# Optimization experiments

Measured on AMD Instinct MI355X. Metric: run time of the kernel, lower is better.

## Reference

```python
import jax, jax.numpy as jnp
import numpy as np

N_NODES = 100000
N_EDGES = 1600000
NEG_SLOPE = 0.2  # PyG GATConv default


def _gat_layer(x, src, dst, W, a_src, a_dst, b, heads, concat):
    """One PyG-style GATConv (eval mode, self-loops already appended)."""
    N = x.shape[0]
    xp = (x @ W).reshape(N, heads, -1)                      # [N, H, C]
    al_s = jnp.einsum('nhc,hc->nh', xp, a_src)              # [N, H]
    al_d = jnp.einsum('nhc,hc->nh', xp, a_dst)              # [N, H]
    e = jax.nn.leaky_relu(al_s[src] + al_d[dst], NEG_SLOPE)  # [E, H]
    # numerically stable segment softmax over incoming edges of each dst
    m = jax.ops.segment_max(e, dst, num_segments=N)         # [N, H]
    ex = jnp.exp(e - m[dst])
    s = jax.ops.segment_sum(ex, dst, num_segments=N)
    alpha = ex / (s[dst] + 1e-16)                           # [E, H]
    out = jax.ops.segment_sum(xp[src] * alpha[:, :, None], dst, num_segments=N)  # [N, H, C]
    out = out.reshape(N, -1) if concat else out.mean(axis=1)
    return out + b


def setup_inputs() -> dict:
    key = jax.random.key(0)
    ks = jax.random.split(key, 16)
    H, C0 = 4, 32  # hidden layers: 4 heads x 32 = 128
    inp = {
        'x': jax.random.normal(ks[0], (N_NODES, 128), dtype=jnp.float32),
        'edge_index': jax.random.randint(ks[1], (2, N_EDGES), 0, N_NODES, dtype=jnp.int64),
        'W0': jax.random.normal(ks[2], (128, 128), dtype=jnp.float32) * 0.1,
        'a_src0': jax.random.normal(ks[3], (H, C0), dtype=jnp.float32) * 0.1,
        'a_dst0': jax.random.normal(ks[4], (H, C0), dtype=jnp.float32) * 0.1,
        'b0': jnp.zeros((128,), dtype=jnp.float32),
        'W1': jax.random.normal(ks[5], (128, 128), dtype=jnp.float32) * 0.1,
        'a_src1': jax.random.normal(ks[6], (H, C0), dtype=jnp.float32) * 0.1,
        'a_dst1': jax.random.normal(ks[7], (H, C0), dtype=jnp.float32) * 0.1,
        'b1': jnp.zeros((128,), dtype=jnp.float32),
        'W2': jax.random.normal(ks[8], (128, 64), dtype=jnp.float32) * 0.1,
        'a_src2': jax.random.normal(ks[9], (1, 64), dtype=jnp.float32) * 0.1,
        'a_dst2': jax.random.normal(ks[10], (1, 64), dtype=jnp.float32) * 0.1,
        'b2': jnp.zeros((64,), dtype=jnp.float32),
    }
    return inp


def reference(x, edge_index, W0, a_src0, a_dst0, b0, W1, a_src1, a_dst1, b1, W2, a_src2, a_dst2, b2):
    N = x.shape[0]
    loop = jnp.arange(N, dtype=edge_index.dtype)
    src = jnp.concatenate([edge_index[0], loop])  # add_self_loops=True
    dst = jnp.concatenate([edge_index[1], loop])
    h = _gat_layer(x, src, dst, W0, a_src0, a_dst0, b0, heads=4, concat=True)
    h = jax.nn.elu(h)
    h = _gat_layer(h, src, dst, W1, a_src1, a_dst1, b1, heads=4, concat=True)
    h = jax.nn.elu(h)
    out = _gat_layer(h, src, dst, W2, a_src2, a_dst2, b2, heads=1, concat=False)
    return out
```

## Files before the change

kernel.cpp:

```cpp
#include <hip/hip_runtime.h>
#include <math.h>


#define N_NODES 100000
#define NBUCK ((N_NODES + 255) / 256)
#define WT_ELEMS (16384 + 16384 + 8192)
#define WT_TOT (WT_ELEMS + NBUCK)

typedef __attribute__((ext_vector_type(4))) _Float16 half4;
typedef __attribute__((ext_vector_type(8))) _Float16 half8;
typedef __attribute__((ext_vector_type(4))) float f32x4;

__device__ inline void fmamix2(float& alo, float& ahi, float s, unsigned u) {
    asm("v_fma_mix_f32 %0, %1, %2, %0 op_sel_hi:[0,1,0]" : "+v"(alo) : "v"(s), "v"(u));
    asm("v_fma_mix_f32 %0, %1, %2, %0 op_sel:[0,1,0] op_sel_hi:[0,1,0]" : "+v"(ahi) : "v"(s), "v"(u));
}


__global__ __launch_bounds__(256) void k_bcount(const int* __restrict__ ei, int E, int ETOT,
                                                int* __restrict__ bucketCnt) {
    __shared__ int h[NBUCK];
    for (int b = threadIdx.x; b < NBUCK; b += 256) h[b] = 0;
    __syncthreads();
    const int base = blockIdx.x * 4096;
#pragma unroll
    for (int j = 0; j < 16; ++j) {
        int idx = base + j * 256 + threadIdx.x;
        if (idx < ETOT) {
            int dst = (idx < E) ? ei[E + idx] : (idx - E);
            atomicAdd(&h[dst >> 8], 1);
        }
    }
    __syncthreads();
    for (int b = threadIdx.x; b < NBUCK; b += 256)
        if (h[b]) atomicAdd(&bucketCnt[b], h[b]);
}

__global__ __launch_bounds__(256) void k_bscan(const int* __restrict__ bucketCnt,
                                               int* __restrict__ bstart,
                                               int* __restrict__ gcur, int ETOT) {
    __shared__ int lds[512];
    const int t = threadIdx.x;
    lds[t] = (t < NBUCK) ? bucketCnt[t] : 0;
    lds[t + 256] = (t + 256 < NBUCK) ? bucketCnt[t + 256] : 0;
    __syncthreads();
    for (int d = 1; d < 512; d <<= 1) {
        int v0 = (t >= d) ? lds[t - d] : 0;
        int v1 = (t + 256 >= d) ? lds[t + 256 - d] : 0;
        __syncthreads();
        lds[t] += v0;
        lds[t + 256] += v1;
        __syncthreads();
    }
    int e0 = (t == 0) ? 0 : lds[t - 1];
    int e1 = lds[t + 255];
    if (t < NBUCK)       { bstart[t] = e0;       gcur[t] = e0; }
    if (t + 256 < NBUCK) { bstart[t + 256] = e1; gcur[t + 256] = e1; }
    if (t == 0) bstart[NBUCK] = ETOT;
}

__global__ __launch_bounds__(256) void k_bplace(const int* __restrict__ ei, int E, int ETOT,
                                                int* __restrict__ gcur, int* __restrict__ tmp) {
    __shared__ int h[NBUCK];
    __shared__ int cur[NBUCK];
    for (int b = threadIdx.x; b < NBUCK; b += 256) h[b] = 0;
    __syncthreads();
    const int base = blockIdx.x * 4096;
    int pk[16], bk[16];
#pragma unroll
    for (int j = 0; j < 16; ++j) {
        int idx = base + j * 256 + threadIdx.x;
        bk[j] = -1;
        if (idx < ETOT) {
            int s, d;
            if (idx < E) { s = ei[idx]; d = ei[E + idx]; }
            else         { s = idx - E; d = idx - E; }
            bk[j] = d >> 8;
            pk[j] = s | ((d & 255) << 17);
            atomicAdd(&h[bk[j]], 1);
        }
    }
    __syncthreads();
    for (int b = threadIdx.x; b < NBUCK; b += 256)
        cur[b] = h[b] ? atomicAdd(&gcur[b], h[b]) : 0;
    __syncthreads();
#pragma unroll
    for (int j = 0; j < 16; ++j) {
        if (bk[j] >= 0) {
            int pos = atomicAdd(&cur[bk[j]], 1);
            tmp[pos] = pk[j];
        }
    }
}

__global__ __launch_bounds__(256) void k_bfinal(const int* __restrict__ tmp,
                                                const int* __restrict__ bstart,
                                                int* __restrict__ rowptr,
                                                int* __restrict__ ssrc, int N) {
    __shared__ int cnt[256];
    __shared__ int cur[256];
    const int t = threadIdx.x;
    const int b = blockIdx.x;
    const int s0 = bstart[b], s1 = bstart[b + 1];
    cnt[t] = 0;
    __syncthreads();
    for (int e = s0 + t; e < s1; e += 256)
        atomicAdd(&cnt[tmp[e] >> 17], 1);
    __syncthreads();
    int c0 = cnt[t];
    for (int d = 1; d < 256; d <<= 1) {
        int v = (t >= d) ? cnt[t - d] : 0;
        __syncthreads();
        cnt[t] += v;
        __syncthreads();
    }
    int excl = cnt[t] - c0;
    int node = b * 256 + t;
    if (node <= N) rowptr[node] = s0 + excl;
    cur[t] = excl;
    __syncthreads();
    for (int e = s0 + t; e < s1; e += 256) {
        int p = tmp[e];
        int pos = atomicAdd(&cur[p >> 17], 1);
        ssrc[s0 + pos] = p & 0x1FFFF;
    }
}

__global__ void k_wt3(const float* __restrict__ W0, const float* __restrict__ W1,
                      const float* __restrict__ W2, _Float16* __restrict__ wt0,
                      _Float16* __restrict__ wt1, _Float16* __restrict__ wt2,
                      int* __restrict__ bucketCnt) {
    int idx = blockIdx.x * 256 + threadIdx.x;
    if (idx < 16384) {
        int k = idx >> 7, n = idx & 127;
        wt0[n * 128 + k] = (_Float16)W0[idx];
    } else if (idx < 32768) {
        int i = idx - 16384;
        int k = i >> 7, n = i & 127;
        wt1[n * 128 + k] = (_Float16)W1[i];
    } else if (idx < WT_ELEMS) {
        int i = idx - 32768;
        int k = i >> 6, n = i & 63;
        wt2[n * 128 + k] = (_Float16)W2[i];
    } else if (idx < WT_TOT) {
        bucketCnt[idx - WT_ELEMS] = 0;
    }
}

template <int OUT, int H, bool INF16>
__global__ __launch_bounds__(256) void k_gemm(const void* __restrict__ Xv_,
                                              const _Float16* __restrict__ Wt,
                                              const float* __restrict__ a_src,
                                              const float* __restrict__ a_dst,
                                              _Float16* __restrict__ XP,
                                              float* __restrict__ al_s,
                                              float* __restrict__ al_d, int N) {
    constexpr int NT = OUT / 16;
    constexpr int C = OUT / H;
    constexpr int LDH = 136;
    __shared__ _Float16 As[64 * LDH];
    __shared__ _Float16 Ws[OUT * LDH];
    const int tid = threadIdx.x;
    const int row0 = blockIdx.x * 64;

    for (int c = tid; c < OUT * 16; c += 256) {
        int r = c >> 4, kc = c & 15;
        *(half8*)&Ws[r * LDH + kc * 8] = *(const half8*)(Wt + r * 128 + kc * 8);
    }
    for (int c = tid; c < 64 * 16; c += 256) {
        int r = c >> 4, kc = c & 15;
        int grow = row0 + r;
        half8 hv;
        if (grow < N) {
            if constexpr (INF16) {
                hv = *(const half8*)((const _Float16*)Xv_ + (size_t)grow * 128 + kc * 8);
            } else {
                const float4* xr = (const float4*)((const float*)Xv_ + (size_t)grow * 128 + kc * 8);
                float4 x0 = xr[0], x1 = xr[1];
                hv[0] = (_Float16)x0.x; hv[1] = (_Float16)x0.y;
                hv[2] = (_Float16)x0.z; hv[3] = (_Float16)x0.w;
                hv[4] = (_Float16)x1.x; hv[5] = (_Float16)x1.y;
                hv[6] = (_Float16)x1.z; hv[7] = (_Float16)x1.w;
            }
        } else {
#pragma unroll
            for (int j = 0; j < 8; ++j) hv[j] = (_Float16)0.f;
        }
        *(half8*)&As[r * LDH + kc * 8] = hv;
    }
    __syncthreads();

    const int w = tid >> 6;
    const int l = tid & 63;
    const int lm = l & 15;
    const int lk = l >> 4;

    f32x4 acc[NT];
#pragma unroll
    for (int nt = 0; nt < NT; ++nt) acc[nt] = {0.f, 0.f, 0.f, 0.f};

#pragma unroll
    for (int ks = 0; ks < 4; ++ks) {
        half8 av = *(const half8*)&As[(w * 16 + lm) * LDH + ks * 32 + lk * 8];
#pragma unroll
        for (int nt = 0; nt < NT; ++nt) {
            half8 bv = *(const half8*)&Ws[(nt * 16 + lm) * LDH + ks * 32 + lk * 8];
            acc[nt] = __builtin_amdgcn_mfma_f32_16x16x32_f16(av, bv, acc[nt], 0, 0, 0);
        }
    }

    float avs[NT], avd[NT];
#pragma unroll
    for (int nt = 0; nt < NT; ++nt) {
        avs[nt] = a_src[nt * 16 + lm];
        avd[nt] = a_dst[nt * 16 + lm];
    }

#pragma unroll
    for (int r = 0; r < 4; ++r) {
        int grow = row0 + w * 16 + lk * 4 + r;
        bool ok = grow < N;
#pragma unroll
        for (int nt = 0; nt < NT; ++nt)
            if (ok) XP[(size_t)grow * OUT + nt * 16 + lm] = (_Float16)acc[nt][r];

        float ps[H], pd[H];
#pragma unroll
        for (int h = 0; h < H; ++h) { ps[h] = 0.f; pd[h] = 0.f; }
#pragma unroll
        for (int nt = 0; nt < NT; ++nt) {
            int h = (nt * 16) / C;
            ps[h] += acc[nt][r] * avs[nt];
            pd[h] += acc[nt][r] * avd[nt];
        }
#pragma unroll
        for (int h = 0; h < H; ++h) {
#pragma unroll
            for (int o = 8; o >= 1; o >>= 1) {
                ps[h] += __shfl_xor(ps[h], o);
                pd[h] += __shfl_xor(pd[h], o);
            }
        }
        if (ok && lm == 0) {
#pragma unroll
            for (int h = 0; h < H; ++h) {
                al_s[(size_t)grow * H + h] = ps[h];
                al_d[(size_t)grow * H + h] = pd[h];
            }
        }
    }
}

template <int OUT, int H, bool ELU, bool OUTF16>
__global__ __launch_bounds__(256) void k_agg(const _Float16* __restrict__ xp,
                                             const float* __restrict__ al_s,
                                             const float* __restrict__ al_d,
                                             const int* __restrict__ rowptr,
                                             const int* __restrict__ ssrc,
                                             const float* __restrict__ bias,
                                             void* __restrict__ out_, int N) {
    constexpr int C = OUT / H;
    constexpr int CPL = OUT / 16;
    const int wid = threadIdx.x >> 6;
    const int lane = threadIdx.x & 63;
    const int qid = lane >> 4;
    const int l4 = lane & 15;
    const int node = blockIdx.x * 4 + wid;
    if (node >= N) return;
    const int rs = rowptr[node];
    const int re = rowptr[node + 1];

    const int c0 = l4 * CPL;
    const int hd = c0 / C;
    const float adh = al_d[(unsigned)node * H + hd];

    float ssum = 0.f;
    float acc[CPL];
#pragma unroll
    for (int j = 0; j < CPL; ++j) acc[j] = 0.f;

    auto edge = [&](int idx) {
        int s = ssrc[idx];
        float e = al_s[(unsigned)s * H + hd] + adh;
        e = e > 0.f ? e : 0.2f * e;
        float a = __expf(e);
        ssum += a;
        unsigned off = (unsigned)s * OUT + c0;
        if constexpr (CPL == 8) {
            uint4 u = *(const uint4*)(xp + off);
            fmamix2(acc[0], acc[1], a, u.x);
            fmamix2(acc[2], acc[3], a, u.y);
            fmamix2(acc[4], acc[5], a, u.z);
            fmamix2(acc[6], acc[7], a, u.w);
        } else {
            uint2 u = *(const uint2*)(xp + off);
            fmamix2(acc[0], acc[1], a, u.x);
            fmamix2(acc[2], acc[3], a, u.y);
        }
    };

    int i = rs;
    for (; i + 16 <= re; i += 16) {
        edge(i + qid); edge(i + qid + 4); edge(i + qid + 8); edge(i + qid + 12);
    }
    for (; i + 8 <= re; i += 8) {
        edge(i + qid); edge(i + qid + 4);
    }
    for (; i + qid < re; i += 4) {
        edge(i + qid);
    }

    ssum += __shfl_xor(ssum, 16);
    ssum += __shfl_xor(ssum, 32);
#pragma unroll
    for (int j = 0; j < CPL; ++j) {
        acc[j] += __shfl_xor(acc[j], 16);
        acc[j] += __shfl_xor(acc[j], 32);
    }

    if (qid == 0) {
        float inv = 1.f / (ssum + 1e-16f);
        float o[CPL];
#pragma unroll
        for (int j = 0; j < CPL; ++j) {
            o[j] = acc[j] * inv + bias[c0 + j];
            if constexpr (ELU) o[j] = o[j] > 0.f ? o[j] : (__expf(o[j]) - 1.f);
        }
        if constexpr (OUTF16) {
            _Float16* op = (_Float16*)out_ + (size_t)node * OUT + c0;
            if constexpr (CPL == 8) {
                half8 hv;
#pragma unroll
                for (int j = 0; j < 8; ++j) hv[j] = (_Float16)o[j];
                *(half8*)op = hv;
            } else {
                half4 hv;
#pragma unroll
                for (int j = 0; j < 4; ++j) hv[j] = (_Float16)o[j];
                *(half4*)op = hv;
            }
        } else {
            float* op = (float*)out_ + (size_t)node * OUT + c0;
            if constexpr (CPL == 8) {
                *(float4*)op = make_float4(o[0], o[1], o[2], o[3]);
                *(float4*)(op + 4) = make_float4(o[4], o[5], o[6], o[7]);
            } else {
                *(float4*)op = make_float4(o[0], o[1], o[2], o[3]);
            }
        }
    }
}


extern "C" void kernel_launch(void* const* d_in, const int* in_sizes, int n_in,
                              void* d_out, int out_size, void* d_ws, size_t ws_size,
                              hipStream_t stream) {
    const int N = N_NODES;
    const float* x     = (const float*)d_in[0];
    const int*   ei    = (const int*)d_in[1];
    const float* W0    = (const float*)d_in[2];
    const float* as0   = (const float*)d_in[3];
    const float* ad0   = (const float*)d_in[4];
    const float* b0    = (const float*)d_in[5];
    const float* W1    = (const float*)d_in[6];
    const float* as1   = (const float*)d_in[7];
    const float* ad1   = (const float*)d_in[8];
    const float* b1    = (const float*)d_in[9];
    const float* W2    = (const float*)d_in[10];
    const float* as2   = (const float*)d_in[11];
    const float* ad2   = (const float*)d_in[12];
    const float* b2    = (const float*)d_in[13];
    float* out = (float*)d_out;

    const int E = in_sizes[1] / 2;
    const int ETOT = E + N;

    char* p = (char*)d_ws;
    auto alloc = [&](size_t bytes) {
        void* r = (void*)p;
        p += (bytes + 255) & ~(size_t)255;
        return r;
    };
    _Float16* xp    = (_Float16*)alloc((size_t)N * 128 * 2);
    _Float16* hbuf  = (_Float16*)alloc((size_t)N * 128 * 2);
    float* als      = (float*)alloc((size_t)N * 4 * 4);
    float* ald      = (float*)alloc((size_t)N * 4 * 4);
    int*   rowptr   = (int*)alloc((size_t)(N + 1) * 4);
    int*   ssrc     = (int*)alloc((size_t)ETOT * 4);
    int*   tmp      = (int*)alloc((size_t)ETOT * 4);
    int*   bucketCnt= (int*)alloc((size_t)NBUCK * 4);
    int*   bstart   = (int*)alloc((size_t)(NBUCK + 1) * 4);
    int*   gcur     = (int*)alloc((size_t)NBUCK * 4);
    _Float16* wt0   = (_Float16*)alloc((size_t)128 * 128 * 2);
    _Float16* wt1   = (_Float16*)alloc((size_t)128 * 128 * 2);
    _Float16* wt2   = (_Float16*)alloc((size_t)128 * 64 * 2);

    k_wt3<<<(WT_TOT + 255) / 256, 256, 0, stream>>>(W0, W1, W2, wt0, wt1, wt2, bucketCnt);

    const int PB = (ETOT + 4095) / 4096;
    k_bcount<<<PB, 256, 0, stream>>>(ei, E, ETOT, bucketCnt);
    k_bscan<<<1, 256, 0, stream>>>(bucketCnt, bstart, gcur, ETOT);
    k_bplace<<<PB, 256, 0, stream>>>(ei, E, ETOT, gcur, tmp);
    k_bfinal<<<NBUCK, 256, 0, stream>>>(tmp, bstart, rowptr, ssrc, N);

    const int gGemm = (N + 63) / 64;
    const int gAgg  = (N + 3) / 4;

    k_gemm<128, 4, false><<<gGemm, 256, 0, stream>>>(x, wt0, as0, ad0, xp, als, ald, N);
    k_agg<128, 4, true, true><<<gAgg, 256, 0, stream>>>(xp, als, ald, rowptr, ssrc, b0, hbuf, N);

    k_gemm<128, 4, true><<<gGemm, 256, 0, stream>>>(hbuf, wt1, as1, ad1, xp, als, ald, N);
    k_agg<128, 4, true, true><<<gAgg, 256, 0, stream>>>(xp, als, ald, rowptr, ssrc, b1, hbuf, N);

    k_gemm<64, 1, true><<<gGemm, 256, 0, stream>>>(hbuf, wt2, as2, ad2, xp, als, ald, N);
    k_agg<64, 1, false, false><<<gAgg, 256, 0, stream>>>(xp, als, ald, rowptr, ssrc, b2, out, N);
}
```

Before: 324.9 us.

## Store projected features in column-slice-major layout and split aggregation per slice

The GEMM now writes XP as 16-column slices, each a contiguous [N,16] array, instead of row-major [N,OUT]. Aggregation launches one block per node group per slice, with each wave handling 32 edges in parallel, two lanes per edge covering 8 halfs each. The aim is a smaller gather working set per launch (each slice is N*32 bytes), which should improve L2 hit rates for random source gathers, and more edge parallelism per node. The cost is that the CSR indices and attention logits are re-read and the exps recomputed once per slice, 8x for hidden layers, and many lanes sit idle for nodes with about 17 edges.

```diff
diff --git a/kernel.cpp b/kernel.cpp
--- a/kernel.cpp
+++ b/kernel.cpp
@@ -222,7 +222,7 @@
         bool ok = grow < N;
 #pragma unroll
         for (int nt = 0; nt < NT; ++nt)
-            if (ok) XP[(size_t)grow * OUT + nt * 16 + lm] = (_Float16)acc[nt][r];
+            if (ok) XP[(size_t)nt * N * 16 + (size_t)grow * 16 + lm] = (_Float16)acc[nt][r];
 
         float ps[H], pd[H];
 #pragma unroll
@@ -259,94 +259,73 @@
                                              const int* __restrict__ ssrc,
                                              const float* __restrict__ bias,
                                              void* __restrict__ out_, int N) {
+    constexpr int SLICES = OUT / 16;
     constexpr int C = OUT / H;
-    constexpr int CPL = OUT / 16;
+    const int slice = blockIdx.x & (SLICES - 1);
+    const int ng = blockIdx.x / SLICES;
     const int wid = threadIdx.x >> 6;
     const int lane = threadIdx.x & 63;
-    const int qid = lane >> 4;
-    const int l4 = lane & 15;
-    const int node = blockIdx.x * 4 + wid;
+    const int el = lane >> 1;
+    const int lh = lane & 1;
+    const int node = ng * 4 + wid;
     if (node >= N) return;
     const int rs = rowptr[node];
     const int re = rowptr[node + 1];
 
-    const int c0 = l4 * CPL;
-    const int hd = c0 / C;
-    const float adh = al_d[(unsigned)node * H + hd];
+    const int head = (H == 1) ? 0 : (slice >> 1);
+    const int c0 = slice * 16 + lh * 8;
+    const float adh = al_d[(unsigned)node * H + head];
+    const _Float16* xps = xp + (size_t)slice * ((size_t)N * 16) + lh * 8;
 
     float ssum = 0.f;
-    float acc[CPL];
-#pragma unroll
-    for (int j = 0; j < CPL; ++j) acc[j] = 0.f;
+    float acc[8];
+#pragma unroll
+    for (int j = 0; j < 8; ++j) acc[j] = 0.f;
 
     auto edge = [&](int idx) {
         int s = ssrc[idx];
-        float e = al_s[(unsigned)s * H + hd] + adh;
+        float e = al_s[(unsigned)s * H + head] + adh;
         e = e > 0.f ? e : 0.2f * e;
         float a = __expf(e);
         ssum += a;
-        unsigned off = (unsigned)s * OUT + c0;
-        if constexpr (CPL == 8) {
-            uint4 u = *(const uint4*)(xp + off);
-            fmamix2(acc[0], acc[1], a, u.x);
-            fmamix2(acc[2], acc[3], a, u.y);
-            fmamix2(acc[4], acc[5], a, u.z);
-            fmamix2(acc[6], acc[7], a, u.w);
-        } else {
-            uint2 u = *(const uint2*)(xp + off);
-            fmamix2(acc[0], acc[1], a, u.x);
-            fmamix2(acc[2], acc[3], a, u.y);
-        }
+        uint4 u = *(const uint4*)(xps + (size_t)s * 16);
+        fmamix2(acc[0], acc[1], a, u.x);
+        fmamix2(acc[2], acc[3], a, u.y);
+        fmamix2(acc[4], acc[5], a, u.z);
+        fmamix2(acc[6], acc[7], a, u.w);
     };
 
     int i = rs;
-    for (; i + 16 <= re; i += 16) {
-        edge(i + qid); edge(i + qid + 4); edge(i + qid + 8); edge(i + qid + 12);
-    }
-    for (; i + 8 <= re; i += 8) {
-        edge(i + qid); edge(i + qid + 4);
-    }
-    for (; i + qid < re; i += 4) {
-        edge(i + qid);
-    }
-
-    ssum += __shfl_xor(ssum, 16);
-    ssum += __shfl_xor(ssum, 32);
-#pragma unroll
-    for (int j = 0; j < CPL; ++j) {
-        acc[j] += __shfl_xor(acc[j], 16);
-        acc[j] += __shfl_xor(acc[j], 32);
-    }
-
-    if (qid == 0) {
+    for (; i + 32 <= re; i += 32) edge(i + el);
+    if (i + el < re) edge(i + el);
+
+#pragma unroll
+    for (int o = 1; o <= 32; o <<= 1) ssum += __shfl_xor(ssum, o);
+    ssum *= 0.5f;
+#pragma unroll
+    for (int j = 0; j < 8; ++j) {
+#pragma unroll
+        for (int o = 2; o <= 32; o <<= 1) acc[j] += __shfl_xor(acc[j], o);
+    }
+
+    if (el == 0) {
         float inv = 1.f / (ssum + 1e-16f);
-        float o[CPL];
-#pragma unroll
-        for (int j = 0; j < CPL; ++j) {
+        float o[8];
+#pragma unroll
+        for (int j = 0; j < 8; ++j) {
             o[j] = acc[j] * inv + bias[c0 + j];
             if constexpr (ELU) o[j] = o[j] > 0.f ? o[j] : (__expf(o[j]) - 1.f);
         }
         if constexpr (OUTF16) {
             _Float16* op = (_Float16*)out_ + (size_t)node * OUT + c0;
-            if constexpr (CPL == 8) {
-                half8 hv;
-#pragma unroll
-                for (int j = 0; j < 8; ++j) hv[j] = (_Float16)o[j];
-                *(half8*)op = hv;
-            } else {
-                half4 hv;
-#pragma unroll
-                for (int j = 0; j < 4; ++j) hv[j] = (_Float16)o[j];
-                *(half4*)op = hv;
-            }
+            half8 hv;
+#pragma unroll
+            for (int j = 0; j < 8; ++j) hv[j] = (_Float16)o[j];
+            *(half8*)op = hv;
         } else {
             float* op = (float*)out_ + (size_t)node * OUT + c0;
-            if constexpr (CPL == 8) {
-                *(float4*)op = make_float4(o[0], o[1], o[2], o[3]);
-                *(float4*)(op + 4) = make_float4(o[4], o[5], o[6], o[7]);
-            } else {
-                *(float4*)op = make_float4(o[0], o[1], o[2], o[3]);
-            }
+            *(float4*)op = make_float4(o[0], o[1], o[2], o[3]);
+            *(float4*)(op + 4) = make_float4(o[4], o[5], o[6], o[7]);
         }
     }
 }
@@ -404,14 +383,14 @@
     k_bfinal<<<NBUCK, 256, 0, stream>>>(tmp, bstart, rowptr, ssrc, N);
 
     const int gGemm = (N + 63) / 64;
-    const int gAgg  = (N + 3) / 4;
+    const int ngrp  = (N + 3) / 4;
 
     k_gemm<128, 4, false><<<gGemm, 256, 0, stream>>>(x, wt0, as0, ad0, xp, als, ald, N);
-    k_agg<128, 4, true, true><<<gAgg, 256, 0, stream>>>(xp, als, ald, rowptr, ssrc, b0, hbuf, N);
+    k_agg<128, 4, true, true><<<ngrp * 8, 256, 0, stream>>>(xp, als, ald, rowptr, ssrc, b0, hbuf, N);
 
     k_gemm<128, 4, true><<<gGemm, 256, 0, stream>>>(hbuf, wt1, as1, ad1, xp, als, ald, N);
-    k_agg<128, 4, true, true><<<gAgg, 256, 0, stream>>>(xp, als, ald, rowptr, ssrc, b1, hbuf, N);
+    k_agg<128, 4, true, true><<<ngrp * 8, 256, 0, stream>>>(xp, als, ald, rowptr, ssrc, b1, hbuf, N);
 
     k_gemm<64, 1, true><<<gGemm, 256, 0, stream>>>(hbuf, wt2, as2, ad2, xp, als, ald, N);
-    k_agg<64, 1, false, false><<<gAgg, 256, 0, stream>>>(xp, als, ald, rowptr, ssrc, b2, out, N);
-}
+    k_agg<64, 1, false, false><<<ngrp * 4, 256, 0, stream>>>(xp, als, ald, rowptr, ssrc, b2, out, N);
+}
```

New measurement: 1.057 ms. 3.25x slower.
